# Kernel optimization log

Hardware: AMD Instinct MI355X
Metric: run time of the kernel (lower is better)

The kernel has to match this reference:

```python
import jax, jax.numpy as jnp
import numpy as np

B = 65536
D = 512
R = 64  # min(64, D) reflections (cap_householder_refl=True)


def setup_inputs() -> dict:
    key = jax.random.key(0)
    k1, k2 = jax.random.split(key)
    x = jax.random.normal(k1, (B, D), dtype=jnp.float32)
    sldj = jnp.zeros((B,), dtype=jnp.float32)
    householder_params = jax.random.normal(k2, (D, R), dtype=jnp.float32)
    return {"x": x, "sldj": sldj, "householder_params": householder_params}


def reference(x, sldj, householder_params):
    # Sequential Householder reflections: x <- x - 2 (x . u_hat) u_hat
    # params: (D, R); unconditioned, so u is shared across the batch.
    us = householder_params.T  # (R, D), scanned in forward order i = 0..R-1

    def step(xc, u):
        unit_u = u / jnp.linalg.norm(u)          # (D,)
        scalar = xc @ unit_u                      # (B,)
        xc = xc - 2.0 * scalar[:, None] * unit_u  # rank-1 update
        return xc, None

    out, _ = jax.lax.scan(step, x, us)
    return out, sldj
```

## Files before the change

### kernel.cpp

```cpp
#include <hip/hip_runtime.h>

typedef __attribute__((ext_vector_type(8))) short bf16x8;
typedef __attribute__((ext_vector_type(4))) float f32x4;

#define DD 512
#define RR 64
#define BTOT 65536
#define BM 128
#define BN 128
#define BK 32

static __device__ __forceinline__ unsigned short f2bf(float f) {
    union { float f; unsigned u; } v; v.f = f;
    unsigned r = v.u + 0x7fffu + ((v.u >> 16) & 1u);
    return (unsigned short)(r >> 16);
}

static __device__ __forceinline__ unsigned pack2bf(float x, float y) {
    union { float f; unsigned u; } a, b;
    a.f = x; b.f = y;
    unsigned ax = a.u + 0x8000u, bx = b.u + 0x8000u;
    return __builtin_amdgcn_perm(bx, ax, 0x07060302u);
}

__global__ void normalize_kernel(const float* __restrict__ P, float* __restrict__ U) {
    int i = blockIdx.x;
    int t = threadIdx.x;
    __shared__ float red[4];
    float a = P[t * RR + i];
    float b = P[(t + 256) * RR + i];
    float p = a * a + b * b;
#pragma unroll
    for (int off = 32; off > 0; off >>= 1) p += __shfl_down(p, off);
    if ((t & 63) == 0) red[t >> 6] = p;
    __syncthreads();
    float s = red[0] + red[1] + red[2] + red[3];
    float inv = 1.0f / sqrtf(s);
    U[i * DD + t]       = a * inv;
    U[i * DD + t + 256] = b * inv;
}

__global__ void compose_kernel(const float* __restrict__ U, unsigned short* __restrict__ Mt) {
    int kb = blockIdx.x * 4;
    int t = threadIdx.x;
    int w = t >> 6;
    __shared__ float red[2][4][4];
    float v0[4], v1[4];
#pragma unroll
    for (int c = 0; c < 4; ++c) {
        v0[c] = (kb + c == t) ? 1.0f : 0.0f;
        v1[c] = (kb + c == t + 256) ? 1.0f : 0.0f;
    }
    float u0n = U[t], u1n = U[t + 256];
    for (int i = 0; i < RR; ++i) {
        float u0 = u0n, u1 = u1n;
        if (i + 1 < RR) { u0n = U[(i + 1) * DD + t]; u1n = U[(i + 1) * DD + t + 256]; }
        float p0 = v0[0] * u0 + v1[0] * u1;
        float p1 = v0[1] * u0 + v1[1] * u1;
        float p2 = v0[2] * u0 + v1[2] * u1;
        float p3 = v0[3] * u0 + v1[3] * u1;
#pragma unroll
        for (int off = 32; off > 0; off >>= 1) {
            p0 += __shfl_down(p0, off);
            p1 += __shfl_down(p1, off);
            p2 += __shfl_down(p2, off);
            p3 += __shfl_down(p3, off);
        }
        if ((t & 63) == 0) {
            red[i & 1][w][0] = p0; red[i & 1][w][1] = p1;
            red[i & 1][w][2] = p2; red[i & 1][w][3] = p3;
        }
        __syncthreads();
        float d[4];
#pragma unroll
        for (int c = 0; c < 4; ++c)
            d[c] = red[i & 1][0][c] + red[i & 1][1][c] + red[i & 1][2][c] + red[i & 1][3][c];
#pragma unroll
        for (int c = 0; c < 4; ++c) {
            v0[c] -= 2.0f * d[c] * u0;
            v1[c] -= 2.0f * d[c] * u1;
        }
    }
#pragma unroll
    for (int c = 0; c < 4; ++c) {
        Mt[(size_t)t * DD + kb + c]         = f2bf(v0[c]);
        Mt[(size_t)(t + 256) * DD + kb + c] = f2bf(v1[c]);
    }
}

__launch_bounds__(256, 4)
__global__ void gemm_kernel(const float* __restrict__ X,
                            const unsigned short* __restrict__ Mt,
                            const float* __restrict__ sldj,
                            float* __restrict__ out) {
    __shared__ __attribute__((aligned(16))) float lAf[BM * BK];
    __shared__ __attribute__((aligned(16))) unsigned short lB[BN * BK];

    int t = threadIdx.x;
    int bid = blockIdx.x;

    if (bid < 64) {
        const float4* s4 = (const float4*)sldj;
        float4* o4 = (float4*)(out + (size_t)BTOT * DD);
        o4[bid * 256 + t] = s4[bid * 256 + t];
    }

    int row_t = (bid >> 5) * 8 + (bid & 7);
    int col_t = (bid >> 3) & 3;
    int row0 = row_t * BM;
    int col0 = col_t * BN;

    int wave = t >> 6, lane = t & 63;
    int wm = wave >> 1, wn = wave & 1;
    int quad = lane >> 4, l16 = lane & 15;

    f32x4 acc[4][4] = {};

    int a_kg = (lane & 7) ^ (lane >> 3);
    int a_mrow = wave * 32 + (lane >> 3);
    int b_kg = (lane & 3) ^ ((lane >> 2) & 3);
    int b_nrow = wave * 32 + (lane >> 2);

    const float* aBase = X + (size_t)(row0 + a_mrow) * DD + a_kg * 4;
    const unsigned short* bBase = Mt + (size_t)(col0 + b_nrow) * DD + b_kg * 8;

#pragma unroll 1
    for (int k0 = 0; k0 < DD; k0 += BK) {
#pragma unroll
        for (int q = 0; q < 4; ++q) {
            const float* g = aBase + k0 + (size_t)q * 8 * DD;
            __builtin_amdgcn_global_load_lds(
                (const __attribute__((address_space(1))) unsigned int*)g,
                (__attribute__((address_space(3))) unsigned int*)(lAf + (wave * 32 + q * 8) * BK),
                16, 0, 0);
        }
#pragma unroll
        for (int q = 0; q < 2; ++q) {
            const unsigned short* g = bBase + k0 + (size_t)q * 16 * DD;
            __builtin_amdgcn_global_load_lds(
                (const __attribute__((address_space(1))) unsigned int*)g,
                (__attribute__((address_space(3))) unsigned int*)(lB + (wave * 32 + q * 16) * BK),
                16, 0, 0);
        }
        __syncthreads();

        bf16x8 bfr[4];
#pragma unroll
        for (int nt = 0; nt < 4; ++nt) {
            int n = wn * 64 + nt * 16 + l16;
            bfr[nt] = *(const bf16x8*)(lB + n * BK + (quad ^ (l16 & 3)) * 8);
        }
#pragma unroll
        for (int mt = 0; mt < 4; ++mt) {
            int m = wm * 64 + mt * 16 + l16;
            int s0 = (2 * quad) ^ (l16 & 7);
            int s1 = (2 * quad + 1) ^ (l16 & 7);
            float4 fa0 = *(const float4*)(lAf + m * BK + s0 * 4);
            float4 fa1 = *(const float4*)(lAf + m * BK + s1 * 4);
            union { unsigned u[4]; bf16x8 v; } afr;
            afr.u[0] = pack2bf(fa0.x, fa0.y);
            afr.u[1] = pack2bf(fa0.z, fa0.w);
            afr.u[2] = pack2bf(fa1.x, fa1.y);
            afr.u[3] = pack2bf(fa1.z, fa1.w);
#pragma unroll
            for (int nt = 0; nt < 4; ++nt)
                acc[mt][nt] = __builtin_amdgcn_mfma_f32_16x16x32_bf16(afr.v, bfr[nt], acc[mt][nt], 0, 0, 0);
        }
        __syncthreads();
    }

#pragma unroll
    for (int mt = 0; mt < 4; ++mt) {
#pragma unroll
        for (int r = 0; r < 4; ++r) {
            int row = row0 + wm * 64 + mt * 16 + quad * 4 + r;
            float* orow = out + (size_t)row * DD + col0 + wn * 64 + l16;
#pragma unroll
            for (int nt = 0; nt < 4; ++nt)
                orow[nt * 16] = acc[mt][nt][r];
        }
    }
}

extern "C" void kernel_launch(void* const* d_in, const int* in_sizes, int n_in,
                              void* d_out, int out_size, void* d_ws, size_t ws_size,
                              hipStream_t stream) {
    const float* x      = (const float*)d_in[0];
    const float* sldj   = (const float*)d_in[1];
    const float* params = (const float*)d_in[2];
    float* out = (float*)d_out;

    float* U = (float*)d_ws;
    unsigned short* Mt = (unsigned short*)((char*)d_ws + RR * DD * sizeof(float));

    normalize_kernel<<<RR, 256, 0, stream>>>(params, U);
    compose_kernel<<<DD / 4, 256, 0, stream>>>(U, Mt);
    gemm_kernel<<<(BTOT / BM) * (DD / BN), 256, 0, stream>>>(x, Mt, sldj, out);
}
```

Baseline: 298.1 us.

## Prefetch A into registers, convert once to bf16 LDS, widen K tile

The GEMM now loads the next fp32 X tile into registers while the MFMAs run on the current one. Each X tile is converted to bf16 once, as it is written to LDS, instead of being repacked by every wave that reads it. The K tile grows to 64, which halves the number of barriers, and occupancy is relaxed to 3 blocks to make room for the registers. The compose kernel is reworked to one wave per column with no LDS reduction, and the sldj copy moves into it.

```diff
diff --git a/kernel.cpp b/kernel.cpp
--- a/kernel.cpp
+++ b/kernel.cpp
@@ -2,13 +2,15 @@
 
 typedef __attribute__((ext_vector_type(8))) short bf16x8;
 typedef __attribute__((ext_vector_type(4))) float f32x4;
+typedef __attribute__((ext_vector_type(4))) unsigned int u32x4;
 
 #define DD 512
 #define RR 64
 #define BTOT 65536
 #define BM 128
 #define BN 128
-#define BK 32
+#define BKT 64
+#define NKT (DD / BKT)
 
 static __device__ __forceinline__ unsigned short f2bf(float f) {
     union { float f; unsigned u; } v; v.f = f;
@@ -40,70 +42,51 @@
     U[i * DD + t + 256] = b * inv;
 }
 
-__global__ void compose_kernel(const float* __restrict__ U, unsigned short* __restrict__ Mt) {
-    int kb = blockIdx.x * 4;
-    int t = threadIdx.x;
-    int w = t >> 6;
-    __shared__ float red[2][4][4];
-    float v0[4], v1[4];
+__global__ void compose_kernel(const float* __restrict__ U,
+                               unsigned short* __restrict__ Mt,
+                               const float* __restrict__ sldj,
+                               float* __restrict__ sldj_out) {
+    int c = blockIdx.x;
+    int l = threadIdx.x;
+
+    ((float2*)sldj_out)[(size_t)c * 64 + l] = ((const float2*)sldj)[(size_t)c * 64 + l];
+
+    float v[8], u[8], un[8];
 #pragma unroll
-    for (int c = 0; c < 4; ++c) {
-        v0[c] = (kb + c == t) ? 1.0f : 0.0f;
-        v1[c] = (kb + c == t + 256) ? 1.0f : 0.0f;
-    }
-    float u0n = U[t], u1n = U[t + 256];
+    for (int j = 0; j < 8; ++j) v[j] = (64 * j + l == c) ? 1.0f : 0.0f;
+#pragma unroll
+    for (int j = 0; j < 8; ++j) u[j] = U[64 * j + l];
+
     for (int i = 0; i < RR; ++i) {
-        float u0 = u0n, u1 = u1n;
-        if (i + 1 < RR) { u0n = U[(i + 1) * DD + t]; u1n = U[(i + 1) * DD + t + 256]; }
-        float p0 = v0[0] * u0 + v1[0] * u1;
-        float p1 = v0[1] * u0 + v1[1] * u1;
-        float p2 = v0[2] * u0 + v1[2] * u1;
-        float p3 = v0[3] * u0 + v1[3] * u1;
+        int inext = (i + 1 < RR) ? i + 1 : i;
 #pragma unroll
-        for (int off = 32; off > 0; off >>= 1) {
-            p0 += __shfl_down(p0, off);
-            p1 += __shfl_down(p1, off);
-            p2 += __shfl_down(p2, off);
-            p3 += __shfl_down(p3, off);
-        }
-        if ((t & 63) == 0) {
-            red[i & 1][w][0] = p0; red[i & 1][w][1] = p1;
-            red[i & 1][w][2] = p2; red[i & 1][w][3] = p3;
-        }
-        __syncthreads();
-        float d[4];
+        for (int j = 0; j < 8; ++j) un[j] = U[inext * DD + 64 * j + l];
+        float s0 = v[0] * u[0] + v[1] * u[1];
+        float s1 = v[2] * u[2] + v[3] * u[3];
+        float s2 = v[4] * u[4] + v[5] * u[5];
+        float s3 = v[6] * u[6] + v[7] * u[7];
+        float s = (s0 + s1) + (s2 + s3);
 #pragma unroll
-        for (int c = 0; c < 4; ++c)
-            d[c] = red[i & 1][0][c] + red[i & 1][1][c] + red[i & 1][2][c] + red[i & 1][3][c];
+        for (int off = 32; off > 0; off >>= 1) s += __shfl_xor(s, off);
+        s *= 2.0f;
 #pragma unroll
-        for (int c = 0; c < 4; ++c) {
-            v0[c] -= 2.0f * d[c] * u0;
-            v1[c] -= 2.0f * d[c] * u1;
-        }
+        for (int j = 0; j < 8; ++j) v[j] -= s * u[j];
+#pragma unroll
+        for (int j = 0; j < 8; ++j) u[j] = un[j];
     }
 #pragma unroll
-    for (int c = 0; c < 4; ++c) {
-        Mt[(size_t)t * DD + kb + c]         = f2bf(v0[c]);
-        Mt[(size_t)(t + 256) * DD + kb + c] = f2bf(v1[c]);
-    }
+    for (int j = 0; j < 8; ++j) Mt[(size_t)(64 * j + l) * DD + c] = f2bf(v[j]);
 }
 
-__launch_bounds__(256, 4)
+__launch_bounds__(256, 3)
 __global__ void gemm_kernel(const float* __restrict__ X,
                             const unsigned short* __restrict__ Mt,
-                            const float* __restrict__ sldj,
                             float* __restrict__ out) {
-    __shared__ __attribute__((aligned(16))) float lAf[BM * BK];
-    __shared__ __attribute__((aligned(16))) unsigned short lB[BN * BK];
+    __shared__ __attribute__((aligned(16))) unsigned short lA[BM * BKT];
+    __shared__ __attribute__((aligned(16))) unsigned short lB[BN * BKT];
 
     int t = threadIdx.x;
     int bid = blockIdx.x;
-
-    if (bid < 64) {
-        const float4* s4 = (const float4*)sldj;
-        float4* o4 = (float4*)(out + (size_t)BTOT * DD);
-        o4[bid * 256 + t] = s4[bid * 256 + t];
-    }
 
     int row_t = (bid >> 5) * 8 + (bid & 7);
     int col_t = (bid >> 3) & 3;
@@ -114,59 +97,75 @@
     int wm = wave >> 1, wn = wave & 1;
     int quad = lane >> 4, l16 = lane & 15;
 
+    int arow = t >> 1, ah = t & 1;
+    const float4* aSrc = (const float4*)(X + (size_t)(row0 + arow) * DD + ah * 32);
+    unsigned short* aDst0 = lA + arow * 64;
+    int s_base = 4 * ah;
+    int arx = arow & 7;
+
+    int bln = lane >> 3;
+    int bg = (lane & 7) ^ bln;
+    const unsigned short* bSrc = Mt + (size_t)(col0 + wave * 32 + bln) * DD + bg * 8;
+
+    const unsigned short* aRd = lA + (wm * 64 + l16) * 64;
+    const unsigned short* bRd = lB + (wn * 64 + l16) * 64;
+    int so0 = (quad ^ (l16 & 7)) * 8;
+    int so1 = ((4 + quad) ^ (l16 & 7)) * 8;
+
     f32x4 acc[4][4] = {};
 
-    int a_kg = (lane & 7) ^ (lane >> 3);
-    int a_mrow = wave * 32 + (lane >> 3);
-    int b_kg = (lane & 3) ^ ((lane >> 2) & 3);
-    int b_nrow = wave * 32 + (lane >> 2);
-
-    const float* aBase = X + (size_t)(row0 + a_mrow) * DD + a_kg * 4;
-    const unsigned short* bBase = Mt + (size_t)(col0 + b_nrow) * DD + b_kg * 8;
+    float4 av[8];
+#pragma unroll
+    for (int j = 0; j < 8; ++j) av[j] = aSrc[j];
 
 #pragma unroll 1
-    for (int k0 = 0; k0 < DD; k0 += BK) {
+    for (int kt = 0; kt < NKT; ++kt) {
+#pragma unroll
+        for (int j4 = 0; j4 < 4; ++j4) {
+            u32x4 wv;
+            float4 x0 = av[2 * j4], x1 = av[2 * j4 + 1];
+            wv.x = pack2bf(x0.x, x0.y);
+            wv.y = pack2bf(x0.z, x0.w);
+            wv.z = pack2bf(x1.x, x1.y);
+            wv.w = pack2bf(x1.z, x1.w);
+            *(u32x4*)(aDst0 + ((s_base + j4) ^ arx) * 8) = wv;
+        }
 #pragma unroll
         for (int q = 0; q < 4; ++q) {
-            const float* g = aBase + k0 + (size_t)q * 8 * DD;
             __builtin_amdgcn_global_load_lds(
-                (const __attribute__((address_space(1))) unsigned int*)g,
-                (__attribute__((address_space(3))) unsigned int*)(lAf + (wave * 32 + q * 8) * BK),
+                (const __attribute__((address_space(1))) unsigned int*)(bSrc + (size_t)q * 8 * DD + kt * BKT),
+                (__attribute__((address_space(3))) unsigned int*)(lB + (wave * 4 + q) * 512),
                 16, 0, 0);
         }
+        __builtin_amdgcn_sched_barrier(0);
+        if (kt + 1 < NKT) {
+            const float4* apn = aSrc + (kt + 1) * (BKT / 4);
 #pragma unroll
-        for (int q = 0; q < 2; ++q) {
-            const unsigned short* g = bBase + k0 + (size_t)q * 16 * DD;
-            __builtin_amdgcn_global_load_lds(
-                (const __attribute__((address_space(1))) unsigned int*)g,
-                (__attribute__((address_space(3))) unsigned int*)(lB + (wave * 32 + q * 16) * BK),
-                16, 0, 0);
+            for (int j = 0; j < 8; ++j) av[j] = apn[j];
+            asm volatile("s_waitcnt vmcnt(8) lgkmcnt(0)" ::: "memory");
+        } else {
+            asm volatile("s_waitcnt vmcnt(0) lgkmcnt(0)" ::: "memory");
         }
-        __syncthreads();
+        __builtin_amdgcn_s_barrier();
+        asm volatile("" ::: "memory");
 
-        bf16x8 bfr[4];
 #pragma unroll
-        for (int nt = 0; nt < 4; ++nt) {
-            int n = wn * 64 + nt * 16 + l16;
-            bfr[nt] = *(const bf16x8*)(lB + n * BK + (quad ^ (l16 & 3)) * 8);
+        for (int sl = 0; sl < 2; ++sl) {
+            int so = sl ? so1 : so0;
+            bf16x8 af[4], bf[4];
+#pragma unroll
+            for (int mt = 0; mt < 4; ++mt) af[mt] = *(const bf16x8*)(aRd + mt * 1024 + so);
+#pragma unroll
+            for (int nt = 0; nt < 4; ++nt) bf[nt] = *(const bf16x8*)(bRd + nt * 1024 + so);
+#pragma unroll
+            for (int mt = 0; mt < 4; ++mt)
+#pragma unroll
+                for (int nt = 0; nt < 4; ++nt)
+                    acc[mt][nt] = __builtin_amdgcn_mfma_f32_16x16x32_bf16(af[mt], bf[nt], acc[mt][nt], 0, 0, 0);
         }
-#pragma unroll
-        for (int mt = 0; mt < 4; ++mt) {
-            int m = wm * 64 + mt * 16 + l16;
-            int s0 = (2 * quad) ^ (l16 & 7);
-            int s1 = (2 * quad + 1) ^ (l16 & 7);
-            float4 fa0 = *(const float4*)(lAf + m * BK + s0 * 4);
-            float4 fa1 = *(const float4*)(lAf + m * BK + s1 * 4);
-            union { unsigned u[4]; bf16x8 v; } afr;
-            afr.u[0] = pack2bf(fa0.x, fa0.y);
-            afr.u[1] = pack2bf(fa0.z, fa0.w);
-            afr.u[2] = pack2bf(fa1.x, fa1.y);
-            afr.u[3] = pack2bf(fa1.z, fa1.w);
-#pragma unroll
-            for (int nt = 0; nt < 4; ++nt)
-                acc[mt][nt] = __builtin_amdgcn_mfma_f32_16x16x32_bf16(afr.v, bfr[nt], acc[mt][nt], 0, 0, 0);
-        }
-        __syncthreads();
+        asm volatile("s_waitcnt lgkmcnt(0)" ::: "memory");
+        __builtin_amdgcn_s_barrier();
+        asm volatile("" ::: "memory");
     }
 
 #pragma unroll
@@ -194,6 +193,6 @@
     unsigned short* Mt = (unsigned short*)((char*)d_ws + RR * DD * sizeof(float));
 
     normalize_kernel<<<RR, 256, 0, stream>>>(params, U);
-    compose_kernel<<<DD / 4, 256, 0, stream>>>(U, Mt);
-    gemm_kernel<<<(BTOT / BM) * (DD / BN), 256, 0, stream>>>(x, Mt, sldj, out);
+    compose_kernel<<<DD, 64, 0, stream>>>(U, Mt, sldj, out + (size_t)BTOT * DD);
+    gemm_kernel<<<(BTOT / BM) * (DD / BN), 256, 0, stream>>>(x, Mt, out);
 }
```

Measured after the change: 300.4 us. About the same (+0.8%).
